# Kernel tuning notes

Hardware: AMD Instinct MI355X
Metric: run time of the kernel (lower is better)

The kernel has to match this reference:

```python
import jax, jax.numpy as jnp
import numpy as np

N_DRUG, N_DIS, E, D = 10000, 15000, 1048576, 128

def setup_inputs() -> dict:
    key = jax.random.key(0)
    k = jax.random.split(key, 6)
    return {
        "z_drug": jax.random.normal(k[0], (N_DRUG, D), dtype=jnp.float32),
        "z_disease": jax.random.normal(k[1], (N_DIS, D), dtype=jnp.float32),
        "row": jax.random.randint(k[2], (E,), 0, N_DRUG),
        "col": jax.random.randint(k[3], (E,), 0, N_DIS),
        "W1": jax.random.normal(k[4], (2 * D, D), dtype=jnp.float32) * (1.0 / np.sqrt(2 * D)),
        "b1": jnp.zeros((D,), dtype=jnp.float32),
        "W2": jax.random.normal(k[5], (D, 1), dtype=jnp.float32) * (1.0 / np.sqrt(D)),
        "b2": jnp.zeros((1,), dtype=jnp.float32),
    }

def reference(z_drug, z_disease, row, col, W1, b1, W2, b2):
    # gather per-edge embeddings and concatenate: [E, 2D]
    z = jnp.concatenate([z_drug[row], z_disease[col]], axis=-1)
    h = jax.nn.relu(z @ W1 + b1)          # [E, D]
    out = h @ W2 + b2                      # [E, 1]
    return out.reshape(-1)                 # [E]
```

## Files before the change

### kernel.cpp

```cpp
#include <hip/hip_runtime.h>

typedef __attribute__((ext_vector_type(8))) short short8;
typedef __attribute__((ext_vector_type(4))) float floatx4;
typedef __attribute__((ext_vector_type(4))) float float4v;
typedef __attribute__((ext_vector_type(4))) unsigned short ushort4v;

#define TILE_M 64
#define TILE_SHORTS (TILE_M * 256)

static __device__ __forceinline__ unsigned short f2bf(float x) {
    unsigned int u = __builtin_bit_cast(unsigned int, x);
    unsigned int r = (u + 0x7FFFu + ((u >> 16) & 1u)) >> 16;
    return (unsigned short)r;
}

static __device__ __forceinline__ void gld16(const unsigned short* g, unsigned short* l) {
    __builtin_amdgcn_global_load_lds(
        (const __attribute__((address_space(1))) unsigned int*)g,
        (__attribute__((address_space(3))) unsigned int*)l, 16, 0, 0);
}

__global__ void prep_all(const float* __restrict__ zd, const float* __restrict__ zs,
                         const float* __restrict__ W1,
                         int nd4, int ns4,
                         unsigned short* __restrict__ outd, unsigned short* __restrict__ outs,
                         unsigned short* __restrict__ w1t) {
    int i = blockIdx.x * 256 + threadIdx.x;
    int total4 = nd4 + ns4;
    if (i < total4) {
        const float* src; unsigned short* dst; int j;
        if (i < nd4) { src = zd; dst = outd; j = i; }
        else         { src = zs; dst = outs; j = i - nd4; }
        float4v v = *reinterpret_cast<const float4v*>(src + (size_t)j * 4);
        ushort4v o;
        o.x = f2bf(v.x); o.y = f2bf(v.y); o.z = f2bf(v.z); o.w = f2bf(v.w);
        *reinterpret_cast<ushort4v*>(dst + (size_t)j * 4) = o;
    } else {
        int j = i - total4;
        if (j < 128 * 256) {
            int n = j >> 8;
            int k = j & 255;
            w1t[n * 256 + k] = f2bf(W1[k * 128 + n]);
        }
    }
}

__global__ __launch_bounds__(256, 2) void edge_mlp(
    const unsigned short* __restrict__ zd, const unsigned short* __restrict__ zs,
    const int* __restrict__ row, const int* __restrict__ col,
    const unsigned short* __restrict__ w1t,
    const float* __restrict__ b1, const float* __restrict__ w2,
    const float* __restrict__ b2, float* __restrict__ out, int ntiles)
{
    __shared__ unsigned short lds_a[2][TILE_SHORTS];
    __shared__ float red[2][2][TILE_M];

    const int tid  = threadIdx.x;
    const int lane = tid & 63;
    const int wave = tid >> 6;
    const int wh   = wave >> 1;
    const int we   = wave & 1;
    const int l15  = lane & 15;
    const int quad = lane >> 4;
    const int whbase = wh * 64;

    short8 wfrag[32];
    #pragma unroll
    for (int s = 0; s < 8; ++s)
        #pragma unroll
        for (int mt = 0; mt < 4; ++mt)
            wfrag[s * 4 + mt] = *reinterpret_cast<const short8*>(
                &w1t[(size_t)(whbase + mt * 16 + l15) * 256 + s * 32 + quad * 8]);

    float4v b1v[4], w2v[4];
    #pragma unroll
    for (int mt = 0; mt < 4; ++mt) {
        b1v[mt] = *reinterpret_cast<const float4v*>(&b1[whbase + mt * 16 + quad * 4]);
        w2v[mt] = *reinterpret_cast<const float4v*>(&w2[whbase + mt * 16 + quad * 4]);
    }
    const float b2v = b2[0];

    const int e0 = tid >> 5;
    const int jxw = tid & 31;
    const int jlog = jxw ^ (e0 & 7);
    const unsigned short* tab = (jlog >= 16) ? zs : zd;
    const int* idxp = (jlog >= 16) ? col : row;
    const int koff = (jlog & 15) * 8;

    const int hb = (l15 >> 2) & 1;
    const int qx = quad ^ (l15 & 3);

    const int G = gridDim.x;
    const int R = ntiles / G;
    const long t0 = blockIdx.x;

    int nidx[8];
    #pragma unroll
    for (int i = 0; i < 8; ++i) nidx[i] = idxp[t0 * TILE_M + e0 + 8 * i];
    #pragma unroll
    for (int i = 0; i < 8; ++i)
        gld16(tab + (size_t)nidx[i] * 128 + koff, &lds_a[0][2048 * i + 512 * wave]);
    {
        long t1 = (R >= 2) ? (t0 + G) : t0;
        #pragma unroll
        for (int i = 0; i < 8; ++i) nidx[i] = idxp[t1 * TILE_M + e0 + 8 * i];
    }

    floatx4 acc[2][4];

    for (int r = 0; r < R; ++r) {
        const long t = t0 + (long)r * G;

        __syncthreads();

        if (r + 1 < R) {
            #pragma unroll
            for (int i = 0; i < 8; ++i)
                gld16(tab + (size_t)nidx[i] * 128 + koff,
                      &lds_a[(r + 1) & 1][2048 * i + 512 * wave]);
        }
        {
            long t2 = (r + 2 < R) ? (t0 + (long)(r + 2) * G) : t0;
            #pragma unroll
            for (int i = 0; i < 8; ++i) nidx[i] = idxp[t2 * TILE_M + e0 + 8 * i];
        }

        if (r >= 2 && lane < 16) {
            int eo = wave * 16 + l15;
            out[(t - 2 * G) * TILE_M + eo] =
                red[r & 1][0][eo] + red[r & 1][1][eo] + b2v;
        }

        if (r >= 1) {
            const int slot = (r - 1) & 1;
            #pragma unroll
            for (int et = 0; et < 2; ++et) {
                float v = 0.f;
                #pragma unroll
                for (int mt = 0; mt < 4; ++mt)
                    #pragma unroll
                    for (int rr = 0; rr < 4; ++rr) {
                        float h = acc[et][mt][rr] + b1v[mt][rr];
                        h = h > 0.f ? h : 0.f;
                        v += h * w2v[mt][rr];
                    }
                v += __shfl_xor(v, 16);
                v += __shfl_xor(v, 32);
                if (lane < 16) red[slot][wh][we * 32 + et * 16 + l15] = v;
            }
        }

        const unsigned short* buf = lds_a[r & 1];
        #pragma unroll
        for (int et = 0; et < 2; ++et)
            #pragma unroll
            for (int mt = 0; mt < 4; ++mt)
                acc[et][mt] = (floatx4)(0.0f);

        #pragma unroll
        for (int s = 0; s < 8; ++s) {
            const int sx = s ^ hb;
            short8 ef[2];
            #pragma unroll
            for (int et = 0; et < 2; ++et) {
                int e = we * 32 + et * 16 + l15;
                ef[et] = *reinterpret_cast<const short8*>(&buf[e * 256 + sx * 32 + qx * 8]);
            }
            #pragma unroll
            for (int et = 0; et < 2; ++et)
                #pragma unroll
                for (int mt = 0; mt < 4; ++mt)
                    acc[et][mt] = __builtin_amdgcn_mfma_f32_16x16x32_bf16(
                        wfrag[s * 4 + mt], ef[et], acc[et][mt], 0, 0, 0);
        }
    }

    __syncthreads();
    if (R >= 2 && lane < 16) {
        int eo = wave * 16 + l15;
        long tt = t0 + (long)(R - 2) * G;
        out[tt * TILE_M + eo] = red[R & 1][0][eo] + red[R & 1][1][eo] + b2v;
    }
    {
        const int slot = (R - 1) & 1;
        #pragma unroll
        for (int et = 0; et < 2; ++et) {
            float v = 0.f;
            #pragma unroll
            for (int mt = 0; mt < 4; ++mt)
                #pragma unroll
                for (int rr = 0; rr < 4; ++rr) {
                    float h = acc[et][mt][rr] + b1v[mt][rr];
                    h = h > 0.f ? h : 0.f;
                    v += h * w2v[mt][rr];
                }
            v += __shfl_xor(v, 16);
            v += __shfl_xor(v, 32);
            if (lane < 16) red[slot][wh][we * 32 + et * 16 + l15] = v;
        }
    }
    __syncthreads();
    if (lane < 16) {
        int eo = wave * 16 + l15;
        long tt = t0 + (long)(R - 1) * G;
        out[tt * TILE_M + eo] = red[(R - 1) & 1][0][eo] + red[(R - 1) & 1][1][eo] + b2v;
    }
}

extern "C" void kernel_launch(void* const* d_in, const int* in_sizes, int n_in,
                              void* d_out, int out_size, void* d_ws, size_t ws_size,
                              hipStream_t stream) {
    const float* zd = (const float*)d_in[0];
    const float* zs = (const float*)d_in[1];
    const int*   row = (const int*)d_in[2];
    const int*   col = (const int*)d_in[3];
    const float* W1 = (const float*)d_in[4];
    const float* b1 = (const float*)d_in[5];
    const float* w2 = (const float*)d_in[6];
    const float* b2 = (const float*)d_in[7];
    float* out = (float*)d_out;

    const int nd = in_sizes[0];
    const int ns = in_sizes[1];
    const int E  = in_sizes[2];

    unsigned short* zd_b = (unsigned short*)d_ws;
    unsigned short* zs_b = zd_b + nd;
    unsigned short* w1t  = zs_b + ns;

    const int total_jobs = (nd + ns) / 4 + 128 * 256;
    const int pgrid = (total_jobs + 255) / 256;
    hipLaunchKernelGGL(prep_all, dim3(pgrid), dim3(256), 0, stream,
                       zd, zs, W1, nd / 4, ns / 4, zd_b, zs_b, w1t);

    const int ntiles = E / TILE_M;
    const int nblocks = 512;
    hipLaunchKernelGGL(edge_mlp, dim3(nblocks), dim3(256), 0, stream,
                       zd_b, zs_b, row, col, w1t, b1, w2, b2, out, ntiles);
}
```

Before: 146.4 us.

## Switch edge MLP to 32x32x16 bf16 MFMA with bias-initialized accumulators

Replaces the 16x16x32 MFMA tiling with 32x32x16 MFMA instructions, so each wave computes a 64x32 output block using two 32x32 accumulators. Edge fragments are loaded once per k-step from LDS with a new XOR swizzle keyed on the edge index. The epilogue needs only one cross-lane shuffle, and b1 is folded into the accumulator initialization instead of being added after the GEMM. The intent is fewer MFMA issues and LDS reads per tile; in exchange the swizzle may cause LDS bank conflicts and the fragment layout must match the 32x32 MFMA operand mapping.

```diff
diff --git a/kernel.cpp b/kernel.cpp
--- a/kernel.cpp
+++ b/kernel.cpp
@@ -1,7 +1,7 @@
 #include <hip/hip_runtime.h>
 
 typedef __attribute__((ext_vector_type(8))) short short8;
-typedef __attribute__((ext_vector_type(4))) float floatx4;
+typedef __attribute__((ext_vector_type(16))) float floatx16;
 typedef __attribute__((ext_vector_type(4))) float float4v;
 typedef __attribute__((ext_vector_type(4))) unsigned short ushort4v;
 
@@ -60,24 +60,26 @@
     const int wave = tid >> 6;
     const int wh   = wave >> 1;
     const int we   = wave & 1;
-    const int l15  = lane & 15;
-    const int quad = lane >> 4;
+    const int l31  = lane & 31;
+    const int h5   = lane >> 5;
     const int whbase = wh * 64;
 
     short8 wfrag[32];
     #pragma unroll
-    for (int s = 0; s < 8; ++s)
-        #pragma unroll
-        for (int mt = 0; mt < 4; ++mt)
-            wfrag[s * 4 + mt] = *reinterpret_cast<const short8*>(
-                &w1t[(size_t)(whbase + mt * 16 + l15) * 256 + s * 32 + quad * 8]);
-
-    float4v b1v[4], w2v[4];
-    #pragma unroll
-    for (int mt = 0; mt < 4; ++mt) {
-        b1v[mt] = *reinterpret_cast<const float4v*>(&b1[whbase + mt * 16 + quad * 4]);
-        w2v[mt] = *reinterpret_cast<const float4v*>(&w2[whbase + mt * 16 + quad * 4]);
-    }
+    for (int s = 0; s < 16; ++s)
+        #pragma unroll
+        for (int mt = 0; mt < 2; ++mt)
+            wfrag[s * 2 + mt] = *reinterpret_cast<const short8*>(
+                &w1t[(size_t)(whbase + mt * 32 + l31) * 256 + s * 16 + h5 * 8]);
+
+    float4v b1i[2][4], w2i[2][4];
+    #pragma unroll
+    for (int mt = 0; mt < 2; ++mt)
+        #pragma unroll
+        for (int g = 0; g < 4; ++g) {
+            b1i[mt][g] = *reinterpret_cast<const float4v*>(&b1[whbase + mt * 32 + g * 8 + h5 * 4]);
+            w2i[mt][g] = *reinterpret_cast<const float4v*>(&w2[whbase + mt * 32 + g * 8 + h5 * 4]);
+        }
     const float b2v = b2[0];
 
     const int e0 = tid >> 5;
@@ -87,8 +89,8 @@
     const int* idxp = (jlog >= 16) ? col : row;
     const int koff = (jlog & 15) * 8;
 
-    const int hb = (l15 >> 2) & 1;
-    const int qx = quad ^ (l15 & 3);
+    const int ecol = we * 32 + l31;
+    const int ek = ecol & 7;
 
     const int G = gridDim.x;
     const int R = ntiles / G;
@@ -106,7 +108,7 @@
         for (int i = 0; i < 8; ++i) nidx[i] = idxp[t1 * TILE_M + e0 + 8 * i];
     }
 
-    floatx4 acc[2][4];
+    floatx16 acc[2];
 
     for (int r = 0; r < R; ++r) {
         const long t = t0 + (long)r * G;
@@ -125,85 +127,71 @@
             for (int i = 0; i < 8; ++i) nidx[i] = idxp[t2 * TILE_M + e0 + 8 * i];
         }
 
-        if (r >= 2 && lane < 16) {
-            int eo = wave * 16 + l15;
-            out[(t - 2 * G) * TILE_M + eo] =
-                red[r & 1][0][eo] + red[r & 1][1][eo] + b2v;
+        if (r >= 2 && tid < TILE_M) {
+            out[(t - 2 * G) * TILE_M + tid] =
+                red[r & 1][0][tid] + red[r & 1][1][tid] + b2v;
         }
 
         if (r >= 1) {
             const int slot = (r - 1) & 1;
-            #pragma unroll
-            for (int et = 0; et < 2; ++et) {
-                float v = 0.f;
+            float v = 0.f;
+            #pragma unroll
+            for (int mt = 0; mt < 2; ++mt)
                 #pragma unroll
-                for (int mt = 0; mt < 4; ++mt)
-                    #pragma unroll
-                    for (int rr = 0; rr < 4; ++rr) {
-                        float h = acc[et][mt][rr] + b1v[mt][rr];
-                        h = h > 0.f ? h : 0.f;
-                        v += h * w2v[mt][rr];
-                    }
-                v += __shfl_xor(v, 16);
-                v += __shfl_xor(v, 32);
-                if (lane < 16) red[slot][wh][we * 32 + et * 16 + l15] = v;
+                for (int rr = 0; rr < 16; ++rr) {
+                    float h = acc[mt][rr];
+                    h = h > 0.f ? h : 0.f;
+                    v += h * w2i[mt][rr >> 2][rr & 3];
+                }
+            v += __shfl_xor(v, 32);
+            if (lane < 32) red[slot][wh][ecol] = v;
+        }
+
+        const unsigned short* buf = lds_a[r & 1];
+        #pragma unroll
+        for (int mt = 0; mt < 2; ++mt)
+            #pragma unroll
+            for (int g = 0; g < 4; ++g) {
+                acc[mt][g * 4 + 0] = b1i[mt][g].x;
+                acc[mt][g * 4 + 1] = b1i[mt][g].y;
+                acc[mt][g * 4 + 2] = b1i[mt][g].z;
+                acc[mt][g * 4 + 3] = b1i[mt][g].w;
             }
-        }
-
-        const unsigned short* buf = lds_a[r & 1];
-        #pragma unroll
-        for (int et = 0; et < 2; ++et)
-            #pragma unroll
-            for (int mt = 0; mt < 4; ++mt)
-                acc[et][mt] = (floatx4)(0.0f);
-
-        #pragma unroll
-        for (int s = 0; s < 8; ++s) {
-            const int sx = s ^ hb;
-            short8 ef[2];
-            #pragma unroll
-            for (int et = 0; et < 2; ++et) {
-                int e = we * 32 + et * 16 + l15;
-                ef[et] = *reinterpret_cast<const short8*>(&buf[e * 256 + sx * 32 + qx * 8]);
-            }
-            #pragma unroll
-            for (int et = 0; et < 2; ++et)
-                #pragma unroll
-                for (int mt = 0; mt < 4; ++mt)
-                    acc[et][mt] = __builtin_amdgcn_mfma_f32_16x16x32_bf16(
-                        wfrag[s * 4 + mt], ef[et], acc[et][mt], 0, 0, 0);
+
+        #pragma unroll
+        for (int s = 0; s < 16; ++s) {
+            short8 ef = *reinterpret_cast<const short8*>(
+                &buf[ecol * 256 + ((s * 2 + h5) ^ ek) * 8]);
+            #pragma unroll
+            for (int mt = 0; mt < 2; ++mt)
+                acc[mt] = __builtin_amdgcn_mfma_f32_32x32x16_bf16(
+                    wfrag[s * 2 + mt], ef, acc[mt], 0, 0, 0);
         }
     }
 
     __syncthreads();
-    if (R >= 2 && lane < 16) {
-        int eo = wave * 16 + l15;
+    if (R >= 2 && tid < TILE_M) {
         long tt = t0 + (long)(R - 2) * G;
-        out[tt * TILE_M + eo] = red[R & 1][0][eo] + red[R & 1][1][eo] + b2v;
+        out[tt * TILE_M + tid] = red[R & 1][0][tid] + red[R & 1][1][tid] + b2v;
     }
     {
         const int slot = (R - 1) & 1;
-        #pragma unroll
-        for (int et = 0; et < 2; ++et) {
-            float v = 0.f;
-            #pragma unroll
-            for (int mt = 0; mt < 4; ++mt)
-                #pragma unroll
-                for (int rr = 0; rr < 4; ++rr) {
-                    float h = acc[et][mt][rr] + b1v[mt][rr];
-                    h = h > 0.f ? h : 0.f;
-                    v += h * w2v[mt][rr];
-                }
-            v += __shfl_xor(v, 16);
-            v += __shfl_xor(v, 32);
-            if (lane < 16) red[slot][wh][we * 32 + et * 16 + l15] = v;
-        }
+        float v = 0.f;
+        #pragma unroll
+        for (int mt = 0; mt < 2; ++mt)
+            #pragma unroll
+            for (int rr = 0; rr < 16; ++rr) {
+                float h = acc[mt][rr];
+                h = h > 0.f ? h : 0.f;
+                v += h * w2i[mt][rr >> 2][rr & 3];
+            }
+        v += __shfl_xor(v, 32);
+        if (lane < 32) red[slot][wh][ecol] = v;
     }
     __syncthreads();
-    if (lane < 16) {
-        int eo = wave * 16 + l15;
+    if (tid < TILE_M) {
         long tt = t0 + (long)(R - 1) * G;
-        out[tt * TILE_M + eo] = red[(R - 1) & 1][0][eo] + red[(R - 1) & 1][1][eo] + b2v;
+        out[tt * TILE_M + tid] = red[(R - 1) & 1][0][tid] + red[(R - 1) & 1][1][tid] + b2v;
     }
 }
 
```

After: 191.4 us. +30.7%, slower.

## Fuse bf16 prep into edge MLP kernel with a grid-wide barrier

Applied to the files above, without the earlier changes.

Removes the separate prep kernel launch by having each of the 512 persistent blocks do a grid-strided share of the bf16 conversion of the embeddings and W1 transpose. A global atomic counter barrier then makes all blocks wait until prep is done before the MLP phase starts. This drops one kernel launch and its tail gap, but adds a memset launch, a spin-wait barrier, and depends on all 512 blocks being resident at the same time, which could deadlock if occupancy is lower than assumed.

```diff
diff --git a/kernel.cpp b/kernel.cpp
--- a/kernel.cpp
+++ b/kernel.cpp
@@ -7,6 +7,7 @@
 
 #define TILE_M 64
 #define TILE_SHORTS (TILE_M * 256)
+#define NBLOCKS 512
 
 static __device__ __forceinline__ unsigned short f2bf(float x) {
     unsigned int u = __builtin_bit_cast(unsigned int, x);
@@ -20,42 +21,60 @@
         (__attribute__((address_space(3))) unsigned int*)l, 16, 0, 0);
 }
 
-__global__ void prep_all(const float* __restrict__ zd, const float* __restrict__ zs,
-                         const float* __restrict__ W1,
-                         int nd4, int ns4,
-                         unsigned short* __restrict__ outd, unsigned short* __restrict__ outs,
-                         unsigned short* __restrict__ w1t) {
-    int i = blockIdx.x * 256 + threadIdx.x;
-    int total4 = nd4 + ns4;
-    if (i < total4) {
-        const float* src; unsigned short* dst; int j;
-        if (i < nd4) { src = zd; dst = outd; j = i; }
-        else         { src = zs; dst = outs; j = i - nd4; }
-        float4v v = *reinterpret_cast<const float4v*>(src + (size_t)j * 4);
-        ushort4v o;
-        o.x = f2bf(v.x); o.y = f2bf(v.y); o.z = f2bf(v.z); o.w = f2bf(v.w);
-        *reinterpret_cast<ushort4v*>(dst + (size_t)j * 4) = o;
-    } else {
-        int j = i - total4;
-        if (j < 128 * 256) {
-            int n = j >> 8;
-            int k = j & 255;
-            w1t[n * 256 + k] = f2bf(W1[k * 128 + n]);
-        }
-    }
-}
-
 __global__ __launch_bounds__(256, 2) void edge_mlp(
-    const unsigned short* __restrict__ zd, const unsigned short* __restrict__ zs,
+    const float* __restrict__ zdf, const float* __restrict__ zsf,
     const int* __restrict__ row, const int* __restrict__ col,
-    const unsigned short* __restrict__ w1t,
+    const float* __restrict__ W1,
     const float* __restrict__ b1, const float* __restrict__ w2,
-    const float* __restrict__ b2, float* __restrict__ out, int ntiles)
+    const float* __restrict__ b2, float* __restrict__ out,
+    unsigned short* __restrict__ zd_b, unsigned short* __restrict__ zs_b,
+    unsigned short* __restrict__ w1t, int* __restrict__ bar,
+    int ntiles, int nd4, int ns4)
 {
     __shared__ unsigned short lds_a[2][TILE_SHORTS];
     __shared__ float red[2][2][TILE_M];
 
     const int tid  = threadIdx.x;
+
+    {
+        const int gtid = blockIdx.x * 256 + tid;
+        const int S = NBLOCKS * 256;
+        const int total4 = nd4 + ns4;
+        const int jobs = total4 + 128 * 256;
+        for (int i = gtid; i < jobs; i += S) {
+            if (i < total4) {
+                const float* src; unsigned short* dst; int j;
+                if (i < nd4) { src = zdf; dst = zd_b; j = i; }
+                else         { src = zsf; dst = zs_b; j = i - nd4; }
+                float4v v = *reinterpret_cast<const float4v*>(src + (size_t)j * 4);
+                ushort4v o;
+                o.x = f2bf(v.x); o.y = f2bf(v.y); o.z = f2bf(v.z); o.w = f2bf(v.w);
+                *reinterpret_cast<ushort4v*>(dst + (size_t)j * 4) = o;
+            } else {
+                int j = i - total4;
+                int n = j >> 8;
+                int k = j & 255;
+                w1t[n * 256 + k] = f2bf(W1[k * 128 + n]);
+            }
+        }
+    }
+
+    __threadfence();
+    __syncthreads();
+    if (tid == 0) {
+        if (atomicAdd(&bar[0], 1) == NBLOCKS - 1) {
+            __hip_atomic_store(&bar[1], 1, __ATOMIC_RELEASE, __HIP_MEMORY_SCOPE_AGENT);
+        } else {
+            while (__hip_atomic_load(&bar[1], __ATOMIC_ACQUIRE, __HIP_MEMORY_SCOPE_AGENT) == 0)
+                __builtin_amdgcn_s_sleep(8);
+        }
+    }
+    __syncthreads();
+    __threadfence();
+
+    const unsigned short* zd = zd_b;
+    const unsigned short* zs = zs_b;
+
     const int lane = tid & 63;
     const int wave = tid >> 6;
     const int wh   = wave >> 1;
@@ -90,7 +109,7 @@
     const int hb = (l15 >> 2) & 1;
     const int qx = quad ^ (l15 & 3);
 
-    const int G = gridDim.x;
+    const int G = NBLOCKS;
     const int R = ntiles / G;
     const long t0 = blockIdx.x;
 
@@ -227,14 +246,14 @@
     unsigned short* zd_b = (unsigned short*)d_ws;
     unsigned short* zs_b = zd_b + nd;
     unsigned short* w1t  = zs_b + ns;
-
-    const int total_jobs = (nd + ns) / 4 + 128 * 256;
-    const int pgrid = (total_jobs + 255) / 256;
-    hipLaunchKernelGGL(prep_all, dim3(pgrid), dim3(256), 0, stream,
-                       zd, zs, W1, nd / 4, ns / 4, zd_b, zs_b, w1t);
-
-    const int ntiles = E / TILE_M;
-    const int nblocks = 512;
-    hipLaunchKernelGGL(edge_mlp, dim3(nblocks), dim3(256), 0, stream,
-                       zd_b, zs_b, row, col, w1t, b1, w2, b2, out, ntiles);
-}
+    int* bar = (int*)(w1t + 128 * 256);
+
+    hipMemsetAsync(bar, 0, 16, stream);
+
+    int ntiles = E / TILE_M;
+    int nd4 = nd / 4, ns4 = ns / 4;
+
+    hipLaunchKernelGGL(edge_mlp, dim3(NBLOCKS), dim3(256), 0, stream,
+                       zd, zs, row, col, W1, b1, w2, b2, out,
+                       zd_b, zs_b, w1t, bar, ntiles, nd4, ns4);
+}
```

Measured after the change: 236.1 us. 61.2% more time.
